# Kernel tuning notes

Hardware: AMD Instinct MI355X
Metric: run time of the kernel (lower is better)

## Reference

```python
import jax, jax.numpy as jnp
import numpy as np

BATCH = 32768
DIM = 256
NUM_LATENTS = 4096
ENTROPY_WEIGHT = 0.1
VQ_BETA = 0.25
EPS = 1e-9


def _l2_normalize(v, axis=-1, eps=1e-12):
    # matches torch F.normalize(dim=-1)
    n = jnp.linalg.norm(v, axis=axis, keepdims=True)
    return v / jnp.maximum(n, eps)


def setup_inputs() -> dict:
    key = jax.random.key(0)
    kx, kc = jax.random.split(key)
    x = jax.random.normal(kx, (BATCH, DIM), dtype=jnp.float32)
    # codebook initialized uniform(-bound, bound) then row-normalized, as in __init__
    bound = (3.0 / DIM) ** 0.5
    cb = jax.random.uniform(kc, (NUM_LATENTS, DIM), dtype=jnp.float32,
                            minval=-bound, maxval=bound)
    codebook = _l2_normalize(cb)
    return {"x": x, "codebook": codebook}


def reference(x, codebook):
    # cosine-distance nearest-code lookup
    x_norm = _l2_normalize(x)                       # [B, D]
    cb_norm = _l2_normalize(codebook)               # [K, D]
    distance = -jnp.einsum('bd,kd->bk', x_norm, cb_norm)  # [B, K]
    # dropout p=0.0 -> identity
    indices = jnp.argmin(distance, axis=-1)         # [B] int
    z = codebook[indices]                           # [B, D] gather

    # straight-through estimator
    z_q = x + jax.lax.stop_gradient(z - x)

    commit_loss = jnp.mean((x - jax.lax.stop_gradient(z)) ** 2)
    q_loss = jnp.mean((z - jax.lax.stop_gradient(x)) ** 2)

    # entropy of codebook usage
    counts = jnp.bincount(indices, length=NUM_LATENTS).astype(jnp.float32)
    probs = counts / counts.sum()
    entropy = -jnp.sum(probs * jnp.log(jnp.clip(probs, EPS)))
    entropy_loss = -entropy

    vq_loss = q_loss + VQ_BETA * commit_loss + ENTROPY_WEIGHT * entropy_loss
    return (z_q, vq_loss, q_loss, commit_loss, entropy_loss, entropy, indices)
```

## Files before the change

### kernel.cpp

```cpp
#include <hip/hip_runtime.h>
#include <math.h>

#define BATCH 32768
#define DIM   256
#define NLAT  4096

typedef _Float16 f16x8 __attribute__((ext_vector_type(8)));
typedef float    f32x16 __attribute__((ext_vector_type(16)));

#define WS_CBH    0u
#define WS_CBINV  2097152u
#define WS_KEYS   2113536u
#define WS_HIST   4210688u

__device__ inline float kdec(uint key) {
  return __uint_as_float(key & 0xFFFFF000u);
}

__global__ __launch_bounds__(256) void prep1_kernel(
    const float* __restrict__ cb, float* __restrict__ cbinv,
    int* __restrict__ hist) {
  int bid = blockIdx.x;
  if (bid < 1024) {
    int w = threadIdx.x >> 6, l = threadIdx.x & 63;
    int row = bid * 4 + w;
    const float4* cr = (const float4*)(cb + (size_t)row * DIM);
    float4 v = cr[l];
    float s = v.x * v.x + v.y * v.y + v.z * v.z + v.w * v.w;
    #pragma unroll
    for (int m = 32; m; m >>= 1) s += __shfl_xor(s, m, 64);
    if (l == 0) cbinv[row] = 1.0f / fmaxf(sqrtf(s), 1e-12f);
  } else {
    for (int k = threadIdx.x; k < NLAT; k += 256) hist[k] = 0;
  }
}

__global__ __launch_bounds__(256) void prep2_kernel(
    const float* __restrict__ x, const float* __restrict__ cb,
    const float* __restrict__ cbinv, uint4* __restrict__ cbhf4,
    uint4* __restrict__ xhf4) {
  int bid = blockIdx.x, tid = threadIdx.x;
  if (bid < 512) {
    int gid = bid * 256 + tid;
    int frag = gid >> 6, lane = gid & 63;
    int rf = frag & 1, ts = frag >> 1, sl = ts & 15, t = ts >> 4;
    int row = t * 64 + rf * 32 + (lane & 31);
    int e4 = sl * 4 + (lane >> 5) * 2;
    const float4* cr = (const float4*)(cb + (size_t)row * DIM);
    float inv = cbinv[row];
    float4 a = cr[e4], b = cr[e4 + 1];
    union { _Float16 h[8]; uint4 u; } pk;
    pk.h[0] = (_Float16)(a.x * inv); pk.h[1] = (_Float16)(a.y * inv);
    pk.h[2] = (_Float16)(a.z * inv); pk.h[3] = (_Float16)(a.w * inv);
    pk.h[4] = (_Float16)(b.x * inv); pk.h[5] = (_Float16)(b.y * inv);
    pk.h[6] = (_Float16)(b.z * inv); pk.h[7] = (_Float16)(b.w * inv);
    cbhf4[gid] = pk.u;
  } else {
    int o = (bid - 512) * 256 + tid;
    int rowgrp = o >> 10, rem = o & 1023;
    int sl = rem >> 6, rem2 = rem & 63;
    int lhh = rem2 >> 5, l31r = rem2 & 31;
    int row = rowgrp * 32 + l31r;
    int c = sl * 2 + lhh;
    const float4* xs = (const float4*)x;
    float4 a = xs[(size_t)row * 64 + c * 2];
    float4 b = xs[(size_t)row * 64 + c * 2 + 1];
    union { _Float16 h[8]; uint4 u; } pk;
    pk.h[0] = (_Float16)a.x; pk.h[1] = (_Float16)a.y;
    pk.h[2] = (_Float16)a.z; pk.h[3] = (_Float16)a.w;
    pk.h[4] = (_Float16)b.x; pk.h[5] = (_Float16)b.y;
    pk.h[6] = (_Float16)b.z; pk.h[7] = (_Float16)b.w;
    xhf4[o] = pk.u;
  }
}

__global__ __launch_bounds__(256, 4) void vq_gemm_kernel(
    const char* __restrict__ xhf, const char* __restrict__ cbhf,
    uint* __restrict__ keys) {
  const int tid = threadIdx.x;
  const int w = tid >> 6, l = tid & 63;
  const int l31 = l & 31, lh = l >> 5;
  const int bb = blockIdx.x >> 2, q = blockIdx.x & 3;
  const int wrow0 = bb * 128 + w * 32;
  const int cbase = q * 1024;
  const uint lh4u = (uint)(lh << 2);

  const char* xb = xhf + ((size_t)(bb * 4 + w) * 1024 + l) * 16;
  f16x8 xf[16];
  #pragma unroll
  for (int s2 = 0; s2 < 16; ++s2) xf[s2] = *(const f16x8*)(xb + s2 * 1024);

  const char* qbase = cbhf + (size_t)q * 524288 + (size_t)l * 16;
  f16x8 ring[4][2];
  #pragma unroll
  for (int s = 0; s < 2; ++s) {
    ring[s][0] = *(const f16x8*)(qbase + s * 2048);
    ring[s][1] = *(const f16x8*)(qbase + s * 2048 + 1024);
  }
  const char* pp = qbase + 4096;

  uint k1 = 0, k2 = 0, k3 = 0;

  #pragma unroll 1
  for (int t = 0; t < 16; ++t) {
    __builtin_amdgcn_s_barrier();
    f32x16 acc[2];
    #pragma unroll
    for (int r = 0; r < 16; ++r) { acc[0][r] = 32.0f; acc[1][r] = 32.0f; }

    #pragma unroll
    for (int sl = 0; sl < 16; ++sl) {
      ring[(sl + 2) & 3][0] = *(const f16x8*)(pp);
      ring[(sl + 2) & 3][1] = *(const f16x8*)(pp + 1024);
      pp += 2048;
      __builtin_amdgcn_s_setprio(1);
      acc[0] = __builtin_amdgcn_mfma_f32_32x32x16_f16(
          ring[sl & 3][0], xf[sl], acc[0], 0, 0, 0);
      acc[1] = __builtin_amdgcn_mfma_f32_32x32x16_f16(
          ring[sl & 3][1], xf[sl], acc[1], 0, 0, 0);
      __builtin_amdgcn_s_setprio(0);
    }

    const uint scode = (uint)(cbase + t * 64);
    #pragma unroll
    for (int rf = 0; rf < 2; ++rf) {
      #pragma unroll
      for (int r = 0; r < 16; ++r) {
        const uint cr = (uint)(rf * 32 + (r & 3) + 8 * (r >> 2));
        uint key = (__float_as_uint(acc[rf][r]) & 0xFFFFF000u)
                 | scode | cr | lh4u;
        uint m1 = max(k1, key), n1 = min(k1, key); k1 = m1;
        uint m2 = max(k2, n1),  n2 = min(k2, n1);  k2 = m2;
        k3 = max(k3, n2);
      }
    }
  }

  uint o1 = __shfl_xor(k1, 32, 64);
  uint o2 = __shfl_xor(k2, 32, 64);
  uint o3 = __shfl_xor(k3, 32, 64);
  uint k4 = 0;
  #pragma unroll
  for (int e = 0; e < 3; ++e) {
    uint o = (e == 0) ? o1 : (e == 1) ? o2 : o3;
    uint m = max(k1, o), n = min(k1, o); k1 = m;
    m = max(k2, n); n = min(k2, n); k2 = m;
    m = max(k3, n); n = min(k3, n); k3 = m;
    k4 = max(k4, n);
  }
  if (lh == 0) {
    uint4 kv; kv.x = k1; kv.y = k2; kv.z = k3; kv.w = k4;
    *(uint4*)(keys + (size_t)(wrow0 + l31) * 16 + q * 4) = kv;
  }
}

__global__ __launch_bounds__(256) void rescore_kernel(
    const float* __restrict__ x, const float* __restrict__ cb,
    const float* __restrict__ cbinv, const uint* __restrict__ keys,
    float* __restrict__ zq, float* __restrict__ out_idx,
    int* __restrict__ hist, double* __restrict__ psse) {
  __shared__ float part[4];
  int tid = threadIdx.x, w = tid >> 6, l = tid & 63;
  int row = blockIdx.x * 4 + w;
  const float4* xr = (const float4*)(x + (size_t)row * DIM);
  float4 xv = xr[l];
  float s0 = xv.x * xv.x + xv.y * xv.y + xv.z * xv.z + xv.w * xv.w;
  #pragma unroll
  for (int m = 32; m; m >>= 1) s0 += __shfl_xor(s0, m, 64);
  float xnorm = sqrtf(s0);
  float xinv = 1.0f / fmaxf(xnorm, 1e-12f);

  uint key = keys[row * 16 + (l & 15)];
  uint kmax = key;
  #pragma unroll
  for (int m = 1; m < 16; m <<= 1) {
    uint o = __shfl_xor(kmax, m, 64);
    kmax = (o > kmax) ? o : kmax;
  }
  float dmax = kdec(kmax);
  float thr = dmax - 2.0f * (3e-3f * xnorm);
  bool inwin = (kdec(key) >= thr) && (l < 16);
  unsigned long long mask = __ballot(inwin);
  int besti;
  if (__popcll(mask) == 1) {
    besti = (int)(kmax & 0xFFFu);
  } else {
    float bestv = -3e38f; besti = 0x7fffffff;
    unsigned long long mm = mask;
    while (mm) {
      int b = __ffsll(mm) - 1; mm &= mm - 1;
      int ci = (int)(__shfl(key, b, 64) & 0xFFFu);
      float cbi = cbinv[ci];
      const float4* cr = (const float4*)(cb + (size_t)ci * DIM);
      float4 cv = cr[l];
      float d = (xv.x * xinv) * (cv.x * cbi) + (xv.y * xinv) * (cv.y * cbi)
              + (xv.z * xinv) * (cv.z * cbi) + (xv.w * xinv) * (cv.w * cbi);
      #pragma unroll
      for (int m = 32; m; m >>= 1) d += __shfl_xor(d, m, 64);
      bool better = (d > bestv) || (d == bestv && ci < besti);
      bestv = better ? d : bestv;
      besti = better ? ci : besti;
    }
  }

  float4 zv = ((const float4*)(cb + (size_t)besti * DIM))[l];
  float4 o;
  o.x = xv.x + (zv.x - xv.x); o.y = xv.y + (zv.y - xv.y);
  o.z = xv.z + (zv.z - xv.z); o.w = xv.w + (zv.w - xv.w);
  ((float4*)(zq + (size_t)row * DIM))[l] = o;
  float dx = xv.x - zv.x, dy = xv.y - zv.y, dz = xv.z - zv.z, dw = xv.w - zv.w;
  float s = dx * dx + dy * dy + dz * dz + dw * dw;
  #pragma unroll
  for (int m = 32; m; m >>= 1) s += __shfl_xor(s, m, 64);
  if (l == 0) part[w] = s;
  __syncthreads();
  if (tid == 0)
    psse[blockIdx.x] = (double)((part[0] + part[1]) + (part[2] + part[3]));
  if (l == 0) {
    atomicAdd(&hist[besti], 1);
    out_idx[row] = (float)besti;
  }
}

__global__ __launch_bounds__(256) void finalize_kernel(
    const int* __restrict__ hist, const double* __restrict__ psse,
    float* __restrict__ outs) {
  int tid = threadIdx.x;
  double e = 0.0, s = 0.0;
  for (int k = tid; k < NLAT; k += 256) {
    int c = hist[k];
    if (c > 0) {
      float p = (float)c * (1.0f / 32768.0f);
      e += (double)(p * logf(p));
    }
  }
  for (int k = tid; k < BATCH / 4; k += 256) s += psse[k];
  #pragma unroll
  for (int off = 32; off; off >>= 1) {
    e += __shfl_xor(e, off, 64);
    s += __shfl_xor(s, off, 64);
  }
  __shared__ double pe[4], ps[4];
  int w = tid >> 6, l = tid & 63;
  if (l == 0) { pe[w] = e; ps[w] = s; }
  __syncthreads();
  if (tid == 0) {
    double H = -((pe[0] + pe[1]) + (pe[2] + pe[3]));
    double sse = (ps[0] + ps[1]) + (ps[2] + ps[3]);
    double qv = sse * (1.0 / ((double)BATCH * (double)DIM));
    float qf = (float)qv;
    float Hf = (float)H;
    float ent_loss = -Hf;
    float vq = qf + 0.25f * qf + 0.1f * ent_loss;
    outs[0] = vq;
    outs[1] = qf;
    outs[2] = qf;
    outs[3] = ent_loss;
    outs[4] = Hf;
  }
}

extern "C" void kernel_launch(void* const* d_in, const int* in_sizes, int n_in,
                              void* d_out, int out_size, void* d_ws, size_t ws_size,
                              hipStream_t stream) {
  const float* x  = (const float*)d_in[0];
  const float* cb = (const float*)d_in[1];

  float* out     = (float*)d_out;
  float* zq      = out;
  float* scalars = out + (size_t)BATCH * DIM;
  float* oidx    = scalars + 5;

  char* wsb = (char*)d_ws;
  ushort* cbhf  = (ushort*)(wsb + WS_CBH);
  float*  cbinv = (float*)(wsb + WS_CBINV);
  uint*   keys  = (uint*)(wsb + WS_KEYS);
  int*    hist  = (int*)(wsb + WS_HIST);
  double* psse  = (double*)(wsb + WS_CBH);

  ushort* xhf = (ushort*)d_out;

  prep1_kernel<<<1025, 256, 0, stream>>>(cb, cbinv, hist);
  prep2_kernel<<<4608, 256, 0, stream>>>(x, cb, cbinv,
                                         (uint4*)cbhf, (uint4*)xhf);
  vq_gemm_kernel<<<1024, 256, 0, stream>>>((const char*)xhf,
                                           (const char*)cbhf, keys);
  rescore_kernel<<<BATCH / 4, 256, 0, stream>>>(x, cb, cbinv, keys,
                                                zq, oidx, hist, psse);
  finalize_kernel<<<1, 256, 0, stream>>>(hist, psse, scalars);
}
```

Measured before the change: 232.2 us.

## Stage codebook tiles through double-buffered LDS via global_load_lds

Codebook fragments used to be streamed from global memory into a per-wave register ring. They are now copied with direct global-to-LDS loads into a 64KB double-buffered shared tile, which all four waves of the block read. This shares codebook traffic across waves and overlaps the next tile's load with the current MFMA work. The cost is a block-wide barrier every tile, LDS read latency inside the MFMA loop, and occupancy cut from 4 to 2 blocks per CU by the large LDS allocation.

After: 201.6 us. 1.15x faster.

```diff
diff --git a/kernel.cpp b/kernel.cpp
--- a/kernel.cpp
+++ b/kernel.cpp
@@ -15,6 +15,12 @@
 
 __device__ inline float kdec(uint key) {
   return __uint_as_float(key & 0xFFFFF000u);
+}
+
+__device__ inline void gload_lds16(const void* g, void* l) {
+  __builtin_amdgcn_global_load_lds(
+      (const __attribute__((address_space(1))) void*)g,
+      (__attribute__((address_space(3))) void*)l, 16, 0, 0);
 }
 
 __global__ __launch_bounds__(256) void prep1_kernel(
@@ -74,9 +80,11 @@
   }
 }
 
-__global__ __launch_bounds__(256, 4) void vq_gemm_kernel(
+__global__ __launch_bounds__(256, 2) void vq_gemm_kernel(
     const char* __restrict__ xhf, const char* __restrict__ cbhf,
     uint* __restrict__ keys) {
+  __shared__ __align__(16) char smem[65536];
+
   const int tid = threadIdx.x;
   const int w = tid >> 6, l = tid & 63;
   const int l31 = l & 31, lh = l >> 5;
@@ -90,35 +98,39 @@
   #pragma unroll
   for (int s2 = 0; s2 < 16; ++s2) xf[s2] = *(const f16x8*)(xb + s2 * 1024);
 
-  const char* qbase = cbhf + (size_t)q * 524288 + (size_t)l * 16;
-  f16x8 ring[4][2];
-  #pragma unroll
-  for (int s = 0; s < 2; ++s) {
-    ring[s][0] = *(const f16x8*)(qbase + s * 2048);
-    ring[s][1] = *(const f16x8*)(qbase + s * 2048 + 1024);
-  }
-  const char* pp = qbase + 4096;
+  const char* qbase = cbhf + (size_t)q * 524288;
+  auto STAGE = [&](int bufoff, int t) {
+    const char* src = qbase + t * 32768 + (size_t)tid * 16;
+    char* dst = smem + bufoff + w * 1024;
+    #pragma unroll
+    for (int s = 0; s < 8; ++s)
+      gload_lds16(src + s * 4096, dst + s * 4096);
+  };
+
+  STAGE(0, 0);
+  asm volatile("s_waitcnt vmcnt(0)" ::: "memory");
+  __syncthreads();
 
   uint k1 = 0, k2 = 0, k3 = 0;
+  int curoff = 0;
 
   #pragma unroll 1
   for (int t = 0; t < 16; ++t) {
-    __builtin_amdgcn_s_barrier();
+    if (t < 15) STAGE(curoff ^ 32768, t + 1);
+
     f32x16 acc[2];
     #pragma unroll
     for (int r = 0; r < 16; ++r) { acc[0][r] = 32.0f; acc[1][r] = 32.0f; }
 
+    const char* bp = smem + curoff + (size_t)l * 16;
     #pragma unroll
     for (int sl = 0; sl < 16; ++sl) {
-      ring[(sl + 2) & 3][0] = *(const f16x8*)(pp);
-      ring[(sl + 2) & 3][1] = *(const f16x8*)(pp + 1024);
-      pp += 2048;
-      __builtin_amdgcn_s_setprio(1);
+      f16x8 a0 = *(const f16x8*)(bp + (sl * 2) * 1024);
+      f16x8 a1 = *(const f16x8*)(bp + (sl * 2 + 1) * 1024);
       acc[0] = __builtin_amdgcn_mfma_f32_32x32x16_f16(
-          ring[sl & 3][0], xf[sl], acc[0], 0, 0, 0);
+          a0, xf[sl], acc[0], 0, 0, 0);
       acc[1] = __builtin_amdgcn_mfma_f32_32x32x16_f16(
-          ring[sl & 3][1], xf[sl], acc[1], 0, 0, 0);
-      __builtin_amdgcn_s_setprio(0);
+          a1, xf[sl], acc[1], 0, 0, 0);
     }
 
     const uint scode = (uint)(cbase + t * 64);
@@ -134,6 +146,10 @@
         k3 = max(k3, n2);
       }
     }
+
+    asm volatile("s_waitcnt vmcnt(0)" ::: "memory");
+    __syncthreads();
+    curoff ^= 32768;
   }
 
   uint o1 = __shfl_xor(k1, 32, 64);
```
